# Optimization experiments

Measured on AMD Instinct MI355X. Metric: run time of the kernel, lower is better.

The kernel has to match this reference:

```python
import jax, jax.numpy as jnp
import numpy as np

SPAN_MAX_LEN = 8
BUCKET_BINS = np.array([0, 1, 2, 3, 4, 5, 7, 8, 15, 16, 31, 32, 63, 64], dtype=np.int64)


def _span_indices(L, max_len):
    # all contiguous spans of width 1..min(L, max_len), grouped by width (matches torch unfold order)
    starts, ends = [], []
    for w in range(1, min(L, max_len) + 1):
        s = np.arange(0, L - w + 1, dtype=np.int64)
        starts.append(s)
        ends.append(s + w - 1)
    return np.concatenate(starts), np.concatenate(ends)


def setup_inputs() -> dict:
    key = jax.random.key(0)
    k1, k2 = jax.random.split(key)
    B, L, D, W = 16, 128, 768, 128
    x = jax.random.normal(k1, (B, L, D), dtype=jnp.float32)
    width_embedding = jax.random.normal(k2, (len(BUCKET_BINS), W), dtype=jnp.float32)
    return {"x": x, "width_embedding": width_embedding, "batch_max_seq_len": L}


def reference(x, width_embedding, batch_max_seq_len):
    B = x.shape[0]
    starts, ends = _span_indices(int(batch_max_seq_len), SPAN_MAX_LEN)  # static np arrays
    widths = ends - starts + 1
    # bucket = last index where width >= bin  ==  searchsorted(side='right') - 1
    buckets = np.searchsorted(BUCKET_BINS, widths, side="right") - 1  # [n_spans]
    n_spans = starts.shape[0]
    hi = x[:, starts, :]                                   # [B, n_spans, D]
    hj = x[:, ends, :]                                     # [B, n_spans, D]
    fw = jnp.broadcast_to(width_embedding[buckets][None, :, :],
                          (B, n_spans, width_embedding.shape[1]))
    spans = jnp.concatenate([hi, hj, fw], axis=-1)         # [B, n_spans, 2D+W]
    span_indices = jnp.stack([jnp.asarray(starts), jnp.asarray(ends)], axis=-1)
    return spans, span_indices
```

## Files before the change

kernel.cpp:

```cpp
#include <hip/hip_runtime.h>


#define LSEQ   128
#define DDIM   768
#define NSPANS 996
#define ROW    1664
#define PER_B  ((long)NSPANS * ROW)
#define XPART_BLOCKS 1536
#define FW_BLOCKS    1992
#define FWTOT        509952
#define IDX4         498
#define SPANS_FLOATS ((long)16 * PER_B)

typedef float f4 __attribute__((ext_vector_type(4)));

__device__ __constant__ int kBase[8] = {0, 128, 255, 381, 506, 630, 753, 875};

__device__ __forceinline__ int bucket_of_span(int s) {
    int w = 1;
    if (s >= 128) w = 2;
    if (s >= 255) w = 3;
    if (s >= 381) w = 4;
    if (s >= 506) w = 5;
    if (s >= 630) w = 6;
    if (s >= 753) w = 7;
    if (s >= 875) w = 8;
    return w - (w >= 6 ? 1 : 0);
}

__device__ __forceinline__ void start_end_of_span(int s, int& start, int& end) {
    int w = 1, base = 0;
    if (s >= 128) { w = 2; base = 128; }
    if (s >= 255) { w = 3; base = 255; }
    if (s >= 381) { w = 4; base = 381; }
    if (s >= 506) { w = 5; base = 506; }
    if (s >= 630) { w = 6; base = 630; }
    if (s >= 753) { w = 7; base = 753; }
    if (s >= 875) { w = 8; base = 875; }
    start = s - base;
    end   = start + w - 1;
}

__global__ __launch_bounds__(256) void span_rep_kernel(
        const float* __restrict__ x,
        const float* __restrict__ we,
        float* __restrict__ out) {
    const int wg = blockIdx.x;

    if (wg < XPART_BLOCKS) {
        const int xcd  = wg & 7;
        const int jj   = wg >> 3;
        const int wave = threadIdx.x >> 6;
        const int lane = threadIdx.x & 63;
        const int gw   = jj * 4 + wave;
        const int half = (gw >= 384) ? 1 : 0;
        const int b    = 2 * xcd + half;
        const int r    = gw - half * 384;
        const int s    = r / 3;
        const int q    = r - s * 3;
        const int c    = (q * 64 + lane) * 4;

        const f4 v = *reinterpret_cast<const f4*>(
            &x[((long)b * LSEQ + s) * DDIM + c]);

        float* ob = out + (long)b * PER_B;

        #pragma unroll
        for (int w = 1; w <= 8; ++w) {
            const int base = (w==1)?0:(w==2)?128:(w==3)?255:(w==4)?381:
                             (w==5)?506:(w==6)?630:(w==7)?753:875;
            if (s <= LSEQ - w) {
                *reinterpret_cast<f4*>(&ob[(long)(base + s) * ROW + c]) = v;
            }
            if (s >= w - 1) {
                *reinterpret_cast<f4*>(&ob[(long)(base + s - w + 1) * ROW + DDIM + c]) = v;
            }
        }
    } else if (wg < XPART_BLOCKS + FW_BLOCKS) {
        const int f = (wg - XPART_BLOCKS) * 256 + (int)threadIdx.x;
        const int b    = f / 31872;
        const int rem  = f - b * 31872;
        const int sIdx = rem >> 5;
        const int c4f  = rem & 31;
        const int bucket = bucket_of_span(sIdx);
        const f4 v = *reinterpret_cast<const f4*>(&we[bucket * 128 + c4f * 4]);
        *reinterpret_cast<f4*>(
            &out[(long)b * PER_B + (long)sIdx * ROW + 2 * DDIM + c4f * 4]) = v;
    } else {
        const int k = (wg - XPART_BLOCKS - FW_BLOCKS) * 256 + (int)threadIdx.x;
        if (k < IDX4) {
            int st0, en0, st1, en1;
            start_end_of_span(2 * k,     st0, en0);
            start_end_of_span(2 * k + 1, st1, en1);
            f4 v = { (float)st0, (float)en0, (float)st1, (float)en1 };
            *reinterpret_cast<f4*>(&out[SPANS_FLOATS + (long)k * 4]) = v;
        }
    }
}

extern "C" void kernel_launch(void* const* d_in, const int* in_sizes, int n_in,
                              void* d_out, int out_size, void* d_ws, size_t ws_size,
                              hipStream_t stream) {
    const float* x  = (const float*)d_in[0];
    const float* we = (const float*)d_in[1];
    float* out = (float*)d_out;

    const int grid = XPART_BLOCKS + FW_BLOCKS + 2;
    span_rep_kernel<<<grid, 256, 0, stream>>>(x, we, out);
}
```

Before: 22.17 us.

## Interleave width-embedding and index work across XCDs by batch locality

```diff
diff --git a/kernel.cpp b/kernel.cpp
--- a/kernel.cpp
+++ b/kernel.cpp
@@ -6,15 +6,18 @@
 #define NSPANS 996
 #define ROW    1664
 #define PER_B  ((long)NSPANS * ROW)
-#define XPART_BLOCKS 1536
-#define FW_BLOCKS    1992
-#define FWTOT        509952
-#define IDX4         498
+
+#define UNITS_HEAVY 768
+#define UNITS_FW    996
+#define UNITS_IDX   4
+#define UNITS_PER_XCD (UNITS_HEAVY + UNITS_FW + UNITS_IDX)
+#define BLOCKS_PER_XCD (UNITS_PER_XCD / 4)
+#define FW_PER_XCD  63744
+#define FW_PER_B    31872
+#define IDX4        498
 #define SPANS_FLOATS ((long)16 * PER_B)
 
 typedef float f4 __attribute__((ext_vector_type(4)));
-
-__device__ __constant__ int kBase[8] = {0, 128, 255, 381, 506, 630, 753, 875};
 
 __device__ __forceinline__ int bucket_of_span(int s) {
     int w = 1;
@@ -45,17 +48,17 @@
         const float* __restrict__ x,
         const float* __restrict__ we,
         float* __restrict__ out) {
-    const int wg = blockIdx.x;
+    const int wg   = blockIdx.x;
+    const int xcd  = wg & 7;
+    const int ublk = wg >> 3;
+    const int wave = threadIdx.x >> 6;
+    const int lane = threadIdx.x & 63;
+    const int unit = ublk * 4 + wave;
 
-    if (wg < XPART_BLOCKS) {
-        const int xcd  = wg & 7;
-        const int jj   = wg >> 3;
-        const int wave = threadIdx.x >> 6;
-        const int lane = threadIdx.x & 63;
-        const int gw   = jj * 4 + wave;
-        const int half = (gw >= 384) ? 1 : 0;
+    if (unit < UNITS_HEAVY) {
+        const int half = (unit >= 384) ? 1 : 0;
         const int b    = 2 * xcd + half;
-        const int r    = gw - half * 384;
+        const int r    = unit - half * 384;
         const int s    = r / 3;
         const int q    = r - s * 3;
         const int c    = (q * 64 + lane) * 4;
@@ -69,17 +72,16 @@
         for (int w = 1; w <= 8; ++w) {
             const int base = (w==1)?0:(w==2)?128:(w==3)?255:(w==4)?381:
                              (w==5)?506:(w==6)?630:(w==7)?753:875;
-            if (s <= LSEQ - w) {
+            if (s <= LSEQ - w)
                 *reinterpret_cast<f4*>(&ob[(long)(base + s) * ROW + c]) = v;
-            }
-            if (s >= w - 1) {
+            if (s >= w - 1)
                 *reinterpret_cast<f4*>(&ob[(long)(base + s - w + 1) * ROW + DDIM + c]) = v;
-            }
         }
-    } else if (wg < XPART_BLOCKS + FW_BLOCKS) {
-        const int f = (wg - XPART_BLOCKS) * 256 + (int)threadIdx.x;
-        const int b    = f / 31872;
-        const int rem  = f - b * 31872;
+    } else if (unit < UNITS_HEAVY + UNITS_FW) {
+        const int fidx = (unit - UNITS_HEAVY) * 64 + lane;
+        const int half = (fidx >= FW_PER_B) ? 1 : 0;
+        const int b    = 2 * xcd + half;
+        const int rem  = fidx - half * FW_PER_B;
         const int sIdx = rem >> 5;
         const int c4f  = rem & 31;
         const int bucket = bucket_of_span(sIdx);
@@ -87,7 +89,7 @@
         *reinterpret_cast<f4*>(
             &out[(long)b * PER_B + (long)sIdx * ROW + 2 * DDIM + c4f * 4]) = v;
     } else {
-        const int k = (wg - XPART_BLOCKS - FW_BLOCKS) * 256 + (int)threadIdx.x;
+        const int k = (xcd * UNITS_IDX + (unit - UNITS_HEAVY - UNITS_FW)) * 64 + lane;
         if (k < IDX4) {
             int st0, en0, st1, en1;
             start_end_of_span(2 * k,     st0, en0);
@@ -105,6 +107,5 @@
     const float* we = (const float*)d_in[1];
     float* out = (float*)d_out;
 
-    const int grid = XPART_BLOCKS + FW_BLOCKS + 2;
-    span_rep_kernel<<<grid, 256, 0, stream>>>(x, we, out);
+    span_rep_kernel<<<8 * BLOCKS_PER_XCD, 256, 0, stream>>>(x, we, out);
 }
```

New measurement: 22.36 us. About the same (+0.8%).
